# Kernel tuning notes

Measured on AMD Instinct MI355X. Metric: run time of the kernel, lower is better.

Reference implementation:

```python
import jax, jax.numpy as jnp
import numpy as np

DIM = 256
HEADS = 8
GH = GW = 8
NTOK = GH * GW            # 64 tokens per window
NW = 49                   # windows per image (56x56 / 8x8)
BATCH = 64
B_ = BATCH * NW           # 3136
POS_DIM = (DIM // 4) // 4 # 16, DynamicPosBias pos_dim
LBIAS = (2 * GH - 1) * (2 * GW - 1)  # 225 relative offsets
EPS = 1e-5


def _ln(x, g, b):
    m = jnp.mean(x, axis=-1, keepdims=True)
    v = jnp.mean((x - m) ** 2, axis=-1, keepdims=True)
    return (x - m) * jax.lax.rsqrt(v + EPS) * g + b


def _make_buffers():
    # biases: all relative (dh, dw) offsets, shape (LBIAS, 2) float
    h = np.arange(1 - GH, GH)
    w = np.arange(1 - GW, GW)
    biases = np.stack(np.meshgrid(h, w, indexing='ij')).reshape(2, -1).T.astype(np.float32)
    # relative_position_index: (NTOK, NTOK) int32 in [0, LBIAS)
    coords = np.stack(np.meshgrid(np.arange(GH), np.arange(GW), indexing='ij')).reshape(2, -1)
    rel = coords[:, :, None] - coords[:, None, :]
    rel = rel.transpose(1, 2, 0).astype(np.int64)
    rel[..., 0] += GH - 1
    rel[..., 1] += GW - 1
    rel[..., 0] *= 2 * GW - 1
    idx = rel.sum(-1).astype(np.int32)
    return jnp.asarray(biases), jnp.asarray(idx)


def setup_inputs() -> dict:
    key = jax.random.key(0)
    ks = iter(jax.random.split(key, 32))
    def w(shape, s=0.02):
        return jax.random.normal(next(ks), shape, jnp.float32) * s
    biases, rel_idx = _make_buffers()
    return {
        'x': jax.random.normal(next(ks), (B_, NTOK, DIM), jnp.float32),
        'mask': jnp.zeros((NW, NTOK, NTOK), jnp.float32),
        'qkv_w': w((3 * DIM, DIM)), 'qkv_b': jnp.zeros((3 * DIM,), jnp.float32),
        'proj_w': w((DIM, DIM)), 'proj_b': jnp.zeros((DIM,), jnp.float32),
        'pos_proj_w': w((POS_DIM, 2)), 'pos_proj_b': jnp.zeros((POS_DIM,), jnp.float32),
        'ln1_g': jnp.ones((POS_DIM,), jnp.float32), 'ln1_b': jnp.zeros((POS_DIM,), jnp.float32),
        'fc1_w': w((POS_DIM, POS_DIM)), 'fc1_b': jnp.zeros((POS_DIM,), jnp.float32),
        'ln2_g': jnp.ones((POS_DIM,), jnp.float32), 'ln2_b': jnp.zeros((POS_DIM,), jnp.float32),
        'fc2_w': w((POS_DIM, POS_DIM)), 'fc2_b': jnp.zeros((POS_DIM,), jnp.float32),
        'ln3_g': jnp.ones((POS_DIM,), jnp.float32), 'ln3_b': jnp.zeros((POS_DIM,), jnp.float32),
        'fc3_w': w((HEADS, POS_DIM)), 'fc3_b': jnp.zeros((HEADS,), jnp.float32),
        'biases': biases, 'rel_idx': rel_idx,
    }


def _forward(x, mask, qkv_w, qkv_b, proj_w, proj_b,
             pos_proj_w, pos_proj_b, ln1_g, ln1_b, fc1_w, fc1_b,
             ln2_g, ln2_b, fc2_w, fc2_b, ln3_g, ln3_b, fc3_w, fc3_b,
             biases, rel_idx):
    Bw, N, C = x.shape
    hd = C // HEADS
    scale = hd ** -0.5
    qkv = (x @ qkv_w.T + qkv_b).reshape(Bw, N, 3, HEADS, hd)
    qkv = jnp.transpose(qkv, (2, 0, 3, 1, 4))  # (3, B_, H, N, hd)
    q, k, v = qkv[0] * scale, qkv[1], qkv[2]
    attn = jnp.einsum('bhnd,bhmd->bhnm', q, k)  # (B_, H, N, N)
    # DynamicPosBias MLP (residual=False): pos3(pos2(pos1(pos_proj(biases))))
    p = biases @ pos_proj_w.T + pos_proj_b
    p = jax.nn.relu(_ln(p, ln1_g, ln1_b)) @ fc1_w.T + fc1_b
    p = jax.nn.relu(_ln(p, ln2_g, ln2_b)) @ fc2_w.T + fc2_b
    p = jax.nn.relu(_ln(p, ln3_g, ln3_b)) @ fc3_w.T + fc3_b  # (LBIAS, H)
    rpb = jnp.transpose(p[rel_idx], (2, 0, 1))  # gather -> (H, N, N)
    attn = attn + rpb[None]
    nW = mask.shape[0]
    attn = attn.reshape(Bw // nW, nW, HEADS, N, N) + mask[None, :, None]
    attn = jax.nn.softmax(attn.reshape(Bw, HEADS, N, N), axis=-1)
    out = jnp.einsum('bhnm,bhmd->bhnd', attn, v)
    out = jnp.transpose(out, (0, 2, 1, 3)).reshape(Bw, N, C)
    return out @ proj_w.T + proj_b


def reference(x, mask, qkv_w, qkv_b, proj_w, proj_b,
              pos_proj_w, pos_proj_b, ln1_g, ln1_b, fc1_w, fc1_b,
              ln2_g, ln2_b, fc2_w, fc2_b, ln3_g, ln3_b, fc3_w, fc3_b,
              biases, rel_idx):
    return _forward(x, mask, qkv_w, qkv_b, proj_w, proj_b,
                    pos_proj_w, pos_proj_b, ln1_g, ln1_b, fc1_w, fc1_b,
                    ln2_g, ln2_b, fc2_w, fc2_b, ln3_g, ln3_b, fc3_w, fc3_b,
                    biases, rel_idx)
```

## Files before the change

### kernel.cpp

```cpp
#include <hip/hip_runtime.h>

#define NTOKS 64
#define DIMS 256
#define NHEADS 8
#define NWIN 49
#define NBLK 3136

typedef __bf16 bf16x8 __attribute__((ext_vector_type(8)));
typedef __bf16 bf16x4 __attribute__((ext_vector_type(4)));
typedef float f32x4 __attribute__((ext_vector_type(4)));

__device__ __forceinline__ unsigned short f2bf(float f) {
    union { float f; unsigned u; } c; c.f = f;
    unsigned u = c.u;
    u += 0x7fffu + ((u >> 16) & 1u);
    return (unsigned short)(u >> 16);
}

__device__ __forceinline__ bf16x8 pack8(f32x4 a, f32x4 b) {
    bf16x8 r;
    r[0] = (__bf16)a[0]; r[1] = (__bf16)a[1];
    r[2] = (__bf16)a[2]; r[3] = (__bf16)a[3];
    r[4] = (__bf16)b[0]; r[5] = (__bf16)b[1];
    r[6] = (__bf16)b[2]; r[7] = (__bf16)b[3];
    return r;
}

template<int NOUT>
__device__ __forceinline__ void ln_relu_fc(const float* v, const float* g, const float* bb,
                                           const float* fw, const float* fb, float* o) {
    float m = 0.f;
#pragma unroll
    for (int j = 0; j < 16; ++j) m += v[j];
    m *= (1.f / 16.f);
    float var = 0.f;
#pragma unroll
    for (int j = 0; j < 16; ++j) { float d = v[j] - m; var += d * d; }
    var *= (1.f / 16.f);
    float inv = rsqrtf(var + 1e-5f);
    float t[16];
#pragma unroll
    for (int j = 0; j < 16; ++j) {
        float xx = (v[j] - m) * inv * g[j] + bb[j];
        t[j] = xx > 0.f ? xx : 0.f;
    }
#pragma unroll
    for (int i = 0; i < NOUT; ++i) {
        float ss = fb[i];
#pragma unroll
        for (int j = 0; j < 16; ++j) ss += fw[i * 16 + j] * t[j];
        o[i] = ss;
    }
}

__global__ void prep_kernel(
    const float* __restrict__ qkv_w, const float* __restrict__ qkv_b,
    const float* __restrict__ proj_w, const float* __restrict__ mask,
    const float* __restrict__ pos_proj_w, const float* __restrict__ pos_proj_b,
    const float* __restrict__ ln1_g, const float* __restrict__ ln1_b,
    const float* __restrict__ fc1_w, const float* __restrict__ fc1_b,
    const float* __restrict__ ln2_g, const float* __restrict__ ln2_b,
    const float* __restrict__ fc2_w, const float* __restrict__ fc2_b,
    const float* __restrict__ ln3_g, const float* __restrict__ ln3_b,
    const float* __restrict__ fc3_w, const float* __restrict__ fc3_b,
    const float* __restrict__ biases, const int* __restrict__ rel_idx,
    unsigned short* __restrict__ qkvw_bf, unsigned short* __restrict__ projw_bf,
    float* __restrict__ qkvb_s, float* __restrict__ rpb_perm,
    float* __restrict__ mask_perm)
{
    const int tid = threadIdx.x;
    const int b = blockIdx.x;
    const float SC = 0.17677669529663687f;

    if (b == 0) {
        __shared__ float p_sh[225 * 8];
        if (tid < 225) {
            float bx = biases[2 * tid], by = biases[2 * tid + 1];
            float v[16], u[16];
#pragma unroll
            for (int j = 0; j < 16; ++j)
                v[j] = pos_proj_w[2 * j] * bx + pos_proj_w[2 * j + 1] * by + pos_proj_b[j];
            ln_relu_fc<16>(v, ln1_g, ln1_b, fc1_w, fc1_b, u);
            ln_relu_fc<16>(u, ln2_g, ln2_b, fc2_w, fc2_b, v);
            ln_relu_fc<8>(v, ln3_g, ln3_b, fc3_w, fc3_b, u);
#pragma unroll
            for (int h = 0; h < 8; ++h) p_sh[tid * 8 + h] = u[h];
        }
        __syncthreads();
        for (int e = tid; e < 32768; e += 256) {
            int r = e & 3, q = (e >> 2) & 63, qd = (e >> 8) & 3, kt = (e >> 10) & 3, h = e >> 12;
            int key = kt * 16 + qd * 4 + r;
            rpb_perm[e] = p_sh[rel_idx[q * 64 + key] * 8 + h];
        }
    } else {
        const int t0 = (b - 1) * 256 + tid, NTH = 127 * 256;
        for (int e = t0; e < 196608; e += NTH) {
            int j = e & 7, lane = (e >> 3) & 63, kk = (e >> 9) & 7, tile = e >> 12;
            int src = (tile * 16 + (lane & 15)) * 256 + kk * 32 + (lane >> 4) * 8 + j;
            float f = qkv_w[src];
            if (src < 65536) f *= SC;
            qkvw_bf[e] = f2bf(f);
        }
        for (int e = t0; e < 65536; e += NTH) {
            int j = e & 7, lane = (e >> 3) & 63, kk = (e >> 9) & 7, tile = e >> 12;
            int src = (tile * 16 + (lane & 15)) * 256 + kk * 32 + (lane >> 4) * 8 + j;
            projw_bf[e] = f2bf(proj_w[src]);
        }
        for (int e = t0; e < 200704; e += NTH) {
            int r = e & 3, q = (e >> 2) & 63, qd = (e >> 8) & 3, kt = (e >> 10) & 3, w = e >> 12;
            int key = kt * 16 + qd * 4 + r;
            mask_perm[e] = mask[w * 4096 + q * 64 + key];
        }
        if (b == 1) {
            for (int e = tid; e < 768; e += 256)
                qkvb_s[e] = qkv_b[e] * (e < 256 ? SC : 1.f);
        }
    }
}

__global__ __launch_bounds__(512, 4) void attn_kernel(
    const float* __restrict__ x,
    const unsigned short* __restrict__ qkvw, const float* __restrict__ qkvb,
    const unsigned short* __restrict__ projw, const float* __restrict__ projb,
    const float* __restrict__ rpb_perm, const float* __restrict__ mask_perm,
    float* __restrict__ out)
{
    __shared__ __align__(16) char ldsb[65536];
    const int tid  = threadIdx.x;
    const int h    = tid >> 6;
    const int lane = tid & 63;
    const int quad = lane >> 4;
    const int l16  = lane & 15;
    const int sw   = (l16 & 7) << 4;
    const int blk  = blockIdx.x;
    const int w    = blk % NWIN;
    const f32x4 FZ = {0.f, 0.f, 0.f, 0.f};

    {
        const float4* xv = (const float4*)(x + (size_t)blk * (NTOKS * DIMS));
#pragma unroll
        for (int it = 0; it < 8; ++it) {
            int i = tid + it * 512;
            float4 f = xv[i];
            int row = i >> 6;
            int colb = (i & 63) << 3;
            bf16x4 hv;
            hv[0] = (__bf16)f.x; hv[1] = (__bf16)f.y;
            hv[2] = (__bf16)f.z; hv[3] = (__bf16)f.w;
            *(bf16x4*)(ldsb + row * 512 + (colb ^ ((row & 7) << 4))) = hv;
        }
    }
    __syncthreads();

    const int xbase = l16 * 512;
#define XFRAG(t, kk) (*(const bf16x8*)(ldsb + (t) * 8192 + xbase + ((((kk) * 64) + quad * 16) ^ sw)))
#define CFRAG(t, kk) (*(const bf16x8*)(ldsb + 32768 + (t) * 8192 + xbase + ((((kk) * 64) + quad * 16) ^ sw)))

    f32x4 qa[2][4], ka[2][4];
#pragma unroll
    for (int mt = 0; mt < 2; ++mt)
#pragma unroll
        for (int nt = 0; nt < 4; ++nt) { qa[mt][nt] = FZ; ka[mt][nt] = FZ; }
    {
        const unsigned short* pQ = qkvw + (size_t)((2 * h) * 8) * 512 + lane * 8;
        const unsigned short* pK = qkvw + (size_t)((16 + 2 * h) * 8) * 512 + lane * 8;
#pragma unroll 2
        for (int kk = 0; kk < 8; ++kk) {
            bf16x8 xb[4];
#pragma unroll
            for (int nt = 0; nt < 4; ++nt) xb[nt] = XFRAG(nt, kk);
            bf16x8 wq[2], wk[2];
#pragma unroll
            for (int mt = 0; mt < 2; ++mt) {
                wq[mt] = *(const bf16x8*)&pQ[(mt * 8 + kk) * 512];
                wk[mt] = *(const bf16x8*)&pK[(mt * 8 + kk) * 512];
            }
#pragma unroll
            for (int mt = 0; mt < 2; ++mt)
#pragma unroll
                for (int nt = 0; nt < 4; ++nt) {
                    qa[mt][nt] = __builtin_amdgcn_mfma_f32_16x16x32_bf16(wq[mt], xb[nt], qa[mt][nt], 0, 0, 0);
                    ka[mt][nt] = __builtin_amdgcn_mfma_f32_16x16x32_bf16(wk[mt], xb[nt], ka[mt][nt], 0, 0, 0);
                }
        }
    }
#pragma unroll
    for (int mt = 0; mt < 2; ++mt) {
        f32x4 qb = *(const f32x4*)&qkvb[h * 32 + mt * 16 + quad * 4];
        f32x4 kb = *(const f32x4*)&qkvb[256 + h * 32 + mt * 16 + quad * 4];
#pragma unroll
        for (int nt = 0; nt < 4; ++nt) {
#pragma unroll
            for (int r = 0; r < 4; ++r) { qa[mt][nt][r] += qb[r]; ka[mt][nt][r] += kb[r]; }
        }
    }
    bf16x8 Qp[4], Kp[4];
#pragma unroll
    for (int t = 0; t < 4; ++t) {
        Qp[t] = pack8(qa[0][t], qa[1][t]);
        Kp[t] = pack8(ka[0][t], ka[1][t]);
    }

    f32x4 s[4][4];
    {
        const f32x4* rp4 = (const f32x4*)rpb_perm + ((h * 16 + quad) * 64 + l16);
        const f32x4* mp4 = (const f32x4*)mask_perm + ((w * 16 + quad) * 64 + l16);
#pragma unroll
        for (int kt = 0; kt < 4; ++kt)
#pragma unroll
            for (int qt = 0; qt < 4; ++qt) {
                f32x4 rv = rp4[kt * 256 + qt * 16];
                f32x4 mv = mp4[kt * 256 + qt * 16];
                s[kt][qt] = rv + mv;
            }
#pragma unroll
        for (int kt = 0; kt < 4; ++kt)
#pragma unroll
            for (int qt = 0; qt < 4; ++qt)
                s[kt][qt] = __builtin_amdgcn_mfma_f32_16x16x32_bf16(Kp[kt], Qp[qt], s[kt][qt], 0, 0, 0);
    }

#pragma unroll
    for (int qt = 0; qt < 4; ++qt) {
        float mx = s[0][qt][0];
#pragma unroll
        for (int kt = 0; kt < 4; ++kt)
#pragma unroll
            for (int r = 0; r < 4; ++r) mx = fmaxf(mx, s[kt][qt][r]);
        mx = fmaxf(mx, __shfl_xor(mx, 16));
        mx = fmaxf(mx, __shfl_xor(mx, 32));
        float sum = 0.f;
#pragma unroll
        for (int kt = 0; kt < 4; ++kt)
#pragma unroll
            for (int r = 0; r < 4; ++r) {
                float e = __expf(s[kt][qt][r] - mx);
                s[kt][qt][r] = e; sum += e;
            }
        sum += __shfl_xor(sum, 16);
        sum += __shfl_xor(sum, 32);
        float inv = 1.0f / sum;
#pragma unroll
        for (int kt = 0; kt < 4; ++kt)
#pragma unroll
            for (int r = 0; r < 4; ++r) s[kt][qt][r] *= inv;
    }
    bf16x8 Pp[4][2];
#pragma unroll
    for (int qt = 0; qt < 4; ++qt)
#pragma unroll
        for (int ks = 0; ks < 2; ++ks)
            Pp[qt][ks] = pack8(s[2 * ks][qt], s[2 * ks + 1][qt]);

    f32x4 va[4][2];
#pragma unroll
    for (int mt = 0; mt < 4; ++mt)
#pragma unroll
        for (int nt = 0; nt < 2; ++nt) va[mt][nt] = FZ;
    {
        const unsigned short* pV = qkvw + (size_t)((32 + 2 * h) * 8) * 512 + lane * 8;
#pragma unroll 2
        for (int kk = 0; kk < 8; ++kk) {
            bf16x8 xa[4];
#pragma unroll
            for (int mt = 0; mt < 4; ++mt) xa[mt] = XFRAG(mt, kk);
            bf16x8 wv[2];
#pragma unroll
            for (int nt = 0; nt < 2; ++nt) wv[nt] = *(const bf16x8*)&pV[(nt * 8 + kk) * 512];
#pragma unroll
            for (int mt = 0; mt < 4; ++mt)
#pragma unroll
                for (int nt = 0; nt < 2; ++nt)
                    va[mt][nt] = __builtin_amdgcn_mfma_f32_16x16x32_bf16(xa[mt], wv[nt], va[mt][nt], 0, 0, 0);
        }
        float vb0 = qkvb[512 + h * 32 + l16];
        float vb1 = qkvb[512 + h * 32 + 16 + l16];
#pragma unroll
        for (int mt = 0; mt < 4; ++mt)
#pragma unroll
            for (int r = 0; r < 4; ++r) { va[mt][0][r] += vb0; va[mt][1][r] += vb1; }
    }
    bf16x8 Vp[2][2];
#pragma unroll
    for (int ks = 0; ks < 2; ++ks)
#pragma unroll
        for (int nt = 0; nt < 2; ++nt)
            Vp[ks][nt] = pack8(va[2 * ks][nt], va[2 * ks + 1][nt]);

    f32x4 o[4][2];
#pragma unroll
    for (int qt = 0; qt < 4; ++qt)
#pragma unroll
        for (int nt = 0; nt < 2; ++nt) {
            f32x4 a0 = __builtin_amdgcn_mfma_f32_16x16x32_bf16(Pp[qt][0], Vp[0][nt], FZ, 0, 0, 0);
            o[qt][nt] = __builtin_amdgcn_mfma_f32_16x16x32_bf16(Pp[qt][1], Vp[1][nt], a0, 0, 0, 0);
        }

    {
        const int chb = 2 * (h * 32 + l16);
#pragma unroll
        for (int qt = 0; qt < 4; ++qt)
#pragma unroll
            for (int r = 0; r < 4; ++r) {
                int row = qt * 16 + quad * 4 + r;
                int rsw = (row & 7) << 4;
#pragma unroll
                for (int nt = 0; nt < 2; ++nt)
                    *(__bf16*)(ldsb + 32768 + row * 512 + ((chb + 32 * nt) ^ rsw)) = (__bf16)o[qt][nt][r];
            }
    }
    __syncthreads();

    {
        f32x4 c_[4][2];
#pragma unroll
        for (int mt = 0; mt < 4; ++mt)
#pragma unroll
            for (int nt = 0; nt < 2; ++nt) c_[mt][nt] = FZ;
        const unsigned short* pP = projw + (size_t)((2 * h) * 8) * 512 + lane * 8;
#pragma unroll 2
        for (int kk = 0; kk < 8; ++kk) {
            bf16x8 a[4];
#pragma unroll
            for (int mt = 0; mt < 4; ++mt) a[mt] = CFRAG(mt, kk);
            bf16x8 bwp[2];
#pragma unroll
            for (int nt = 0; nt < 2; ++nt) bwp[nt] = *(const bf16x8*)&pP[(nt * 8 + kk) * 512];
#pragma unroll
            for (int mt = 0; mt < 4; ++mt)
#pragma unroll
                for (int nt = 0; nt < 2; ++nt)
                    c_[mt][nt] = __builtin_amdgcn_mfma_f32_16x16x32_bf16(a[mt], bwp[nt], c_[mt][nt], 0, 0, 0);
        }
        float pb0 = projb[h * 32 + l16];
        float pb1 = projb[h * 32 + 16 + l16];
        float* ob = out + (size_t)blk * (NTOKS * DIMS) + h * 32 + l16;
#pragma unroll
        for (int mt = 0; mt < 4; ++mt)
#pragma unroll
            for (int r = 0; r < 4; ++r) {
                int row = mt * 16 + quad * 4 + r;
                ob[row * 256]      = c_[mt][0][r] + pb0;
                ob[row * 256 + 16] = c_[mt][1][r] + pb1;
            }
    }
#undef XFRAG
#undef CFRAG
}

extern "C" void kernel_launch(void* const* d_in, const int* in_sizes, int n_in,
                              void* d_out, int out_size, void* d_ws, size_t ws_size,
                              hipStream_t stream) {
    const float* x          = (const float*)d_in[0];
    const float* mask       = (const float*)d_in[1];
    const float* qkv_w      = (const float*)d_in[2];
    const float* qkv_b      = (const float*)d_in[3];
    const float* proj_w     = (const float*)d_in[4];
    const float* proj_b     = (const float*)d_in[5];
    const float* pos_proj_w = (const float*)d_in[6];
    const float* pos_proj_b = (const float*)d_in[7];
    const float* ln1_g      = (const float*)d_in[8];
    const float* ln1_b      = (const float*)d_in[9];
    const float* fc1_w      = (const float*)d_in[10];
    const float* fc1_b      = (const float*)d_in[11];
    const float* ln2_g      = (const float*)d_in[12];
    const float* ln2_b      = (const float*)d_in[13];
    const float* fc2_w      = (const float*)d_in[14];
    const float* fc2_b      = (const float*)d_in[15];
    const float* ln3_g      = (const float*)d_in[16];
    const float* ln3_b      = (const float*)d_in[17];
    const float* fc3_w      = (const float*)d_in[18];
    const float* fc3_b      = (const float*)d_in[19];
    const float* biases     = (const float*)d_in[20];
    const int*   rel_idx    = (const int*)d_in[21];
    float* out = (float*)d_out;

    char* ws = (char*)d_ws;
    unsigned short* qkvw_bf  = (unsigned short*)(ws);
    unsigned short* projw_bf = (unsigned short*)(ws + 393216);
    float* qkvb_s    = (float*)(ws + 524288);
    float* rpb_perm  = (float*)(ws + 528384);
    float* mask_perm = (float*)(ws + 659456);

    prep_kernel<<<dim3(128), dim3(256), 0, stream>>>(
        qkv_w, qkv_b, proj_w, mask, pos_proj_w, pos_proj_b,
        ln1_g, ln1_b, fc1_w, fc1_b, ln2_g, ln2_b, fc2_w, fc2_b,
        ln3_g, ln3_b, fc3_w, fc3_b, biases, rel_idx,
        qkvw_bf, projw_bf, qkvb_s, rpb_perm, mask_perm);

    attn_kernel<<<dim3(NBLK), dim3(512), 0, stream>>>(
        x, qkvw_bf, qkvb_s, projw_bf, proj_b, rpb_perm, mask_perm, out);
}
```

Baseline: 517.5 us.

## Halve LDS by reusing x buffer for attention output, transpose MFMAs for vector stores

The attention output is now staged in the same LDS region as the bf16 x tile, with an extra barrier, so the shared buffer drops from 64 KB to 32 KB and more workgroups can fit per CU. The PV and projection MFMAs swap operand order so results land transposed, which allows 8-byte LDS writes and float4 global stores in place of scalar stores. MFMA sections are also wrapped in s_setprio to favour matrix issue. The cost is an additional __syncthreads before the buffer is overwritten.

```diff
diff --git a/kernel.cpp b/kernel.cpp
--- a/kernel.cpp
+++ b/kernel.cpp
@@ -125,7 +125,7 @@
     const float* __restrict__ rpb_perm, const float* __restrict__ mask_perm,
     float* __restrict__ out)
 {
-    __shared__ __align__(16) char ldsb[65536];
+    __shared__ __align__(16) char ldsb[32768];
     const int tid  = threadIdx.x;
     const int h    = tid >> 6;
     const int lane = tid & 63;
@@ -154,7 +154,6 @@
 
     const int xbase = l16 * 512;
 #define XFRAG(t, kk) (*(const bf16x8*)(ldsb + (t) * 8192 + xbase + ((((kk) * 64) + quad * 16) ^ sw)))
-#define CFRAG(t, kk) (*(const bf16x8*)(ldsb + 32768 + (t) * 8192 + xbase + ((((kk) * 64) + quad * 16) ^ sw)))
 
     f32x4 qa[2][4], ka[2][4];
 #pragma unroll
@@ -175,6 +174,7 @@
                 wq[mt] = *(const bf16x8*)&pQ[(mt * 8 + kk) * 512];
                 wk[mt] = *(const bf16x8*)&pK[(mt * 8 + kk) * 512];
             }
+            __builtin_amdgcn_s_setprio(1);
 #pragma unroll
             for (int mt = 0; mt < 2; ++mt)
 #pragma unroll
@@ -182,6 +182,7 @@
                     qa[mt][nt] = __builtin_amdgcn_mfma_f32_16x16x32_bf16(wq[mt], xb[nt], qa[mt][nt], 0, 0, 0);
                     ka[mt][nt] = __builtin_amdgcn_mfma_f32_16x16x32_bf16(wk[mt], xb[nt], ka[mt][nt], 0, 0, 0);
                 }
+            __builtin_amdgcn_s_setprio(0);
         }
     }
 #pragma unroll
@@ -213,11 +214,13 @@
                 f32x4 mv = mp4[kt * 256 + qt * 16];
                 s[kt][qt] = rv + mv;
             }
+        __builtin_amdgcn_s_setprio(1);
 #pragma unroll
         for (int kt = 0; kt < 4; ++kt)
 #pragma unroll
             for (int qt = 0; qt < 4; ++qt)
                 s[kt][qt] = __builtin_amdgcn_mfma_f32_16x16x32_bf16(Kp[kt], Qp[qt], s[kt][qt], 0, 0, 0);
+        __builtin_amdgcn_s_setprio(0);
     }
 
 #pragma unroll
@@ -267,11 +270,13 @@
             bf16x8 wv[2];
 #pragma unroll
             for (int nt = 0; nt < 2; ++nt) wv[nt] = *(const bf16x8*)&pV[(nt * 8 + kk) * 512];
+            __builtin_amdgcn_s_setprio(1);
 #pragma unroll
             for (int mt = 0; mt < 4; ++mt)
 #pragma unroll
                 for (int nt = 0; nt < 2; ++nt)
                     va[mt][nt] = __builtin_amdgcn_mfma_f32_16x16x32_bf16(xa[mt], wv[nt], va[mt][nt], 0, 0, 0);
+            __builtin_amdgcn_s_setprio(0);
         }
         float vb0 = qkvb[512 + h * 32 + l16];
         float vb1 = qkvb[512 + h * 32 + 16 + l16];
@@ -287,65 +292,73 @@
         for (int nt = 0; nt < 2; ++nt)
             Vp[ks][nt] = pack8(va[2 * ks][nt], va[2 * ks + 1][nt]);
 
-    f32x4 o[4][2];
-#pragma unroll
-    for (int qt = 0; qt < 4; ++qt)
-#pragma unroll
-        for (int nt = 0; nt < 2; ++nt) {
-            f32x4 a0 = __builtin_amdgcn_mfma_f32_16x16x32_bf16(Pp[qt][0], Vp[0][nt], FZ, 0, 0, 0);
-            o[qt][nt] = __builtin_amdgcn_mfma_f32_16x16x32_bf16(Pp[qt][1], Vp[1][nt], a0, 0, 0, 0);
-        }
-
-    {
-        const int chb = 2 * (h * 32 + l16);
-#pragma unroll
-        for (int qt = 0; qt < 4; ++qt)
-#pragma unroll
-            for (int r = 0; r < 4; ++r) {
-                int row = qt * 16 + quad * 4 + r;
-                int rsw = (row & 7) << 4;
-#pragma unroll
-                for (int nt = 0; nt < 2; ++nt)
-                    *(__bf16*)(ldsb + 32768 + row * 512 + ((chb + 32 * nt) ^ rsw)) = (__bf16)o[qt][nt][r];
+    __syncthreads();
+
+    f32x4 o2[2][4];
+    __builtin_amdgcn_s_setprio(1);
+#pragma unroll
+    for (int nt = 0; nt < 2; ++nt)
+#pragma unroll
+        for (int qt = 0; qt < 4; ++qt) {
+            f32x4 a0 = __builtin_amdgcn_mfma_f32_16x16x32_bf16(Vp[0][nt], Pp[qt][0], FZ, 0, 0, 0);
+            o2[nt][qt] = __builtin_amdgcn_mfma_f32_16x16x32_bf16(Vp[1][nt], Pp[qt][1], a0, 0, 0, 0);
+        }
+    __builtin_amdgcn_s_setprio(0);
+
+    {
+#pragma unroll
+        for (int qt = 0; qt < 4; ++qt) {
+            char* rowp = ldsb + qt * 8192 + xbase;
+#pragma unroll
+            for (int nt = 0; nt < 2; ++nt) {
+                bf16x4 hv;
+                hv[0] = (__bf16)o2[nt][qt][0];
+                hv[1] = (__bf16)o2[nt][qt][1];
+                hv[2] = (__bf16)o2[nt][qt][2];
+                hv[3] = (__bf16)o2[nt][qt][3];
+                *(bf16x4*)(rowp + ((64 * h + 32 * nt + 8 * quad) ^ sw)) = hv;
             }
+        }
     }
     __syncthreads();
 
     {
-        f32x4 c_[4][2];
-#pragma unroll
-        for (int mt = 0; mt < 4; ++mt)
-#pragma unroll
-            for (int nt = 0; nt < 2; ++nt) c_[mt][nt] = FZ;
+        f32x4 c2[2][4];
+#pragma unroll
+        for (int ot = 0; ot < 2; ++ot)
+#pragma unroll
+            for (int qt = 0; qt < 4; ++qt) c2[ot][qt] = FZ;
         const unsigned short* pP = projw + (size_t)((2 * h) * 8) * 512 + lane * 8;
 #pragma unroll 2
         for (int kk = 0; kk < 8; ++kk) {
-            bf16x8 a[4];
-#pragma unroll
-            for (int mt = 0; mt < 4; ++mt) a[mt] = CFRAG(mt, kk);
+            bf16x8 cb[4];
+#pragma unroll
+            for (int qt = 0; qt < 4; ++qt) cb[qt] = XFRAG(qt, kk);
             bf16x8 bwp[2];
 #pragma unroll
-            for (int nt = 0; nt < 2; ++nt) bwp[nt] = *(const bf16x8*)&pP[(nt * 8 + kk) * 512];
-#pragma unroll
-            for (int mt = 0; mt < 4; ++mt)
-#pragma unroll
-                for (int nt = 0; nt < 2; ++nt)
-                    c_[mt][nt] = __builtin_amdgcn_mfma_f32_16x16x32_bf16(a[mt], bwp[nt], c_[mt][nt], 0, 0, 0);
-        }
-        float pb0 = projb[h * 32 + l16];
-        float pb1 = projb[h * 32 + 16 + l16];
-        float* ob = out + (size_t)blk * (NTOKS * DIMS) + h * 32 + l16;
-#pragma unroll
-        for (int mt = 0; mt < 4; ++mt)
-#pragma unroll
-            for (int r = 0; r < 4; ++r) {
-                int row = mt * 16 + quad * 4 + r;
-                ob[row * 256]      = c_[mt][0][r] + pb0;
-                ob[row * 256 + 16] = c_[mt][1][r] + pb1;
+            for (int ot = 0; ot < 2; ++ot) bwp[ot] = *(const bf16x8*)&pP[(ot * 8 + kk) * 512];
+            __builtin_amdgcn_s_setprio(1);
+#pragma unroll
+            for (int ot = 0; ot < 2; ++ot)
+#pragma unroll
+                for (int qt = 0; qt < 4; ++qt)
+                    c2[ot][qt] = __builtin_amdgcn_mfma_f32_16x16x32_bf16(bwp[ot], cb[qt], c2[ot][qt], 0, 0, 0);
+            __builtin_amdgcn_s_setprio(0);
+        }
+        f32x4 pb[2];
+#pragma unroll
+        for (int ot = 0; ot < 2; ++ot)
+            pb[ot] = *(const f32x4*)&projb[h * 32 + ot * 16 + quad * 4];
+        float* ob = out + (size_t)blk * (NTOKS * DIMS);
+#pragma unroll
+        for (int qt = 0; qt < 4; ++qt)
+#pragma unroll
+            for (int ot = 0; ot < 2; ++ot) {
+                f32x4 v = c2[ot][qt] + pb[ot];
+                *(float4*)&ob[(qt * 16 + l16) * 256 + h * 32 + ot * 16 + quad * 4] = *(float4*)&v;
             }
     }
 #undef XFRAG
-#undef CFRAG
 }
 
 extern "C" void kernel_launch(void* const* d_in, const int* in_sizes, int n_in,
```

After: 550.7 us. +6.4%, slower.
